# Kernel optimization log

Hardware: AMD Instinct MI355X
Metric: run time of the kernel (lower is better)

Reference implementation:

```python
import jax, jax.numpy as jnp
import numpy as np

# QP per sample: minimize c^T x + L2_REG * ||x||^2  s.t.  A x = b, lb <= x <= ub
# Solved with ADMM (splitting x = z, z in box), which is the differentiable-through-
# unrolling analogue of the SCS conic solve in the original CvxpyLayer.
L2_REG = 0.1   # config['l2_reg']
RHO = 1.0      # ADMM penalty
N_ITERS = 100  # fixed unrolled iteration count (config['diff_solver_iters'] scaled down)
JITTER = 1e-5

B, M_DIM, N_DIM = 32768, 16, 32


def setup_inputs() -> dict:
    key = jax.random.key(0)
    kA, kx, kc, kl, ku = jax.random.split(key, 5)
    A = jax.random.normal(kA, (B, M_DIM, N_DIM), jnp.float32) / np.sqrt(N_DIM)
    # feasible anchor point so the QP always has a solution
    x0 = jax.random.uniform(kx, (B, N_DIM), jnp.float32, -1.0, 1.0)
    b = jnp.einsum('bmn,bn->bm', A, x0)
    c = jax.random.normal(kc, (B, N_DIM), jnp.float32)
    lb = x0 - jax.random.uniform(kl, (B, N_DIM), jnp.float32, 0.5, 1.5)
    ub = x0 + jax.random.uniform(ku, (B, N_DIM), jnp.float32, 0.5, 1.5)
    return {"A": A, "b": b, "c": c, "lb": lb, "ub": ub}


def _solve_qp(A, b, c, lb, ub):
    sigma = 2.0 * L2_REG + RHO  # Hessian of x-subproblem is sigma*I
    m = A.shape[-2]
    # Gram matrix A A^T, inverted once per sample (small: m x m)
    M = jnp.einsum('bmn,bkn->bmk', A, A) + JITTER * jnp.eye(m, dtype=A.dtype)
    Minv = jnp.linalg.inv(M)

    def step(state, _):
        x, z, u = state
        v = RHO * (z - u) - c
        # equality-constrained x-update via KKT: x = (v - A^T nu)/sigma with A x = b
        rhs = jnp.einsum('bmn,bn->bm', A, v) - sigma * b
        nu = jnp.einsum('bmk,bk->bm', Minv, rhs)
        x = (v - jnp.einsum('bmn,bm->bn', A, nu)) / sigma
        z = jnp.clip(x + u, lb, ub)
        u = u + x - z
        return (x, z, u), None

    z0 = jnp.clip(jnp.zeros_like(c), lb, ub)
    init = (jnp.zeros_like(c), z0, jnp.zeros_like(c))
    (x, z, u), _ = jax.lax.scan(step, init, None, length=N_ITERS)
    return x


def reference(A, b, c, lb, ub):
    return _solve_qp(A, b, c, lb, ub)
```

## Files before the change

### kernel.cpp

```cpp
#include <hip/hip_runtime.h>

typedef float f16v __attribute__((ext_vector_type(16)));
typedef float f4 __attribute__((ext_vector_type(4)));
typedef float f2 __attribute__((ext_vector_type(2)));

template<int I> struct ic { static constexpr int v = I; };
template<int... I> struct iseq {};
template<int N, int... I> struct mk : mk<N-1, N-1, I...> {};
template<int... I> struct mk<0, I...> { using t = iseq<I...>; };
template<class F, int... I>
__device__ __forceinline__ void sfor_impl(F f, iseq<I...>) { (f(ic<I>{}), ...); }
template<int N, class F>
__device__ __forceinline__ void sfor(F f) { sfor_impl(f, typename mk<N>::t{}); }

namespace {
constexpr float kSigma  = 1.2f;
constexpr float kJitter = 1e-5f;
constexpr int   kIters  = 100;
constexpr int   MD = 16;
constexpr int   ND = 32;
constexpr int   SPA = 8;
constexpr int   AS  = 132;
}

__device__ __forceinline__ float4 lds_a4(const float* As, int r, int j) {
    return *reinterpret_cast<const float4*>(&As[r * 32 + ((j ^ (r & 7)) << 2)]);
}
__device__ __forceinline__ f2 lds_a2(const float* As, int r, int n) {
    return *reinterpret_cast<const f2*>(
        &As[r * 32 + ((((n >> 2) ^ (r & 7)) << 2) | (n & 3))]);
}

__global__ void __launch_bounds__(128)
admm_fused_kernel(const float* __restrict__ Ag, const float* __restrict__ bg,
                  const float* __restrict__ cg, const float* __restrict__ lbg,
                  const float* __restrict__ ubg, float* __restrict__ outg)
{
    __shared__ __align__(16) float A_lds[SPA * AS * 4];

    const int t = threadIdx.x;

    {
        const float4* src = reinterpret_cast<const float4*>(Ag) +
                            (size_t)blockIdx.x * (SPA * MD * ND / 4);
        float4* dst = reinterpret_cast<float4*>(A_lds);
        #pragma unroll
        for (int r = 0; r < 8; ++r) {
            int idx = r * 128 + t;
            int smp = idx >> 7;
            int row = (idx >> 3) & 15;
            int j   = idx & 7;
            dst[smp * AS + row * 8 + (j ^ (row & 7))] = src[idx];
        }
    }
    __syncthreads();

    const int lane = t & 63;
    const int l    = lane & 15;
    const int n0   = 2 * l;
    const int smp  = (t >> 6) * 4 + (lane >> 4);
    const size_t gs = (size_t)blockIdx.x * SPA + smp;
    const float* As = &A_lds[smp * AS * 4];

    f16v Ar0, Ar1;
    sfor<4>([&](auto J) {
        constexpr int j = decltype(J)::v;
        float4 v  = lds_a4(As, l, j);
        Ar0[4*j+0] = v.x;  Ar0[4*j+1] = v.y;  Ar0[4*j+2] = v.z;  Ar0[4*j+3] = v.w;
        float4 w4 = lds_a4(As, l, j + 4);
        Ar1[4*j+0] = w4.x; Ar1[4*j+1] = w4.y; Ar1[4*j+2] = w4.z; Ar1[4*j+3] = w4.w;
    });

    f16v Mrow, Vrow;
    sfor<16>([&](auto K) {
        constexpr int k = decltype(K)::v;
        float a0 = 0.f, a1 = 0.f, a2 = 0.f, a3 = 0.f;
        sfor<4>([&](auto J) {
            constexpr int j = decltype(J)::v;
            float4 v  = lds_a4(As, k, j);
            a0 += Ar0[4*j+0]*v.x;  a1 += Ar0[4*j+1]*v.y;
            a2 += Ar0[4*j+2]*v.z;  a3 += Ar0[4*j+3]*v.w;
            float4 w4 = lds_a4(As, k, j + 4);
            a0 += Ar1[4*j+0]*w4.x; a1 += Ar1[4*j+1]*w4.y;
            a2 += Ar1[4*j+2]*w4.z; a3 += Ar1[4*j+3]*w4.w;
        });
        Mrow[k] = (a0+a1)+(a2+a3) + ((k == l) ? kJitter : 0.f);
        Vrow[k] = (k == l) ? 1.f : 0.f;
    });

    sfor<16>([&](auto K) {
        constexpr int k = decltype(K)::v;
        float ip = 1.f / __shfl(Mrow[k], k, 16);
        float f  = (l == k) ? 0.f : Mrow[k] * ip;
        sfor<16>([&](auto J) {
            constexpr int j = decltype(J)::v;
            if constexpr (j > k) {
                float mj = __shfl(Mrow[j], k, 16);
                Mrow[j] = (l == k) ? mj * ip : Mrow[j] - f * mj;
            }
        });
        sfor<16>([&](auto J) {
            constexpr int j = decltype(J)::v;
            if constexpr (j < k) {
                float vj = __shfl(Vrow[j], k, 16);
                Vrow[j] = (l == k) ? vj * ip : Vrow[j] - f * vj;
            }
        });
        Vrow[k] = (l == k) ? ip : -f;
    });

    float w = 0.f;
    {
        float bval = bg[gs * MD + l];
        sfor<16>([&](auto K) {
            constexpr int k = decltype(K)::v;
            w += Vrow[k] * __shfl(bval, k, 16);
        });
    }

    f16v Ca = (f16v)0.0f, Cb = (f16v)0.0f;
    float q0 = 0.f, q1 = 0.f;
    sfor<16>([&](auto K) {
        constexpr int k = decltype(K)::v;
        f2 ak = lds_a2(As, k, n0);
        float wm = __shfl(w, k, 16);
        q0 = fmaf(ak[0], wm, q0);
        q1 = fmaf(ak[1], wm, q1);
        sfor<16>([&](auto M) {
            constexpr int m = decltype(M)::v;
            float mv = __shfl(Vrow[m], k, 16);
            Ca[m] = fmaf(ak[0], mv, Ca[m]);
            Cb[m] = fmaf(ak[1], mv, Cb[m]);
        });
    });

    constexpr float is = 1.f / kSigma;
#define QBUILD(j)                                                             \
    f2 Qa##j, Qb##j;                                                          \
    {                                                                         \
        const int n = 2 * ((l - (j)) & 15);                                   \
        float qa0 = 0.f, qa1 = 0.f, qb0 = 0.f, qb1 = 0.f;                     \
        sfor<16>([&](auto M) {                                                \
            constexpr int m = decltype(M)::v;                                 \
            f2 ak = lds_a2(As, m, n);                                         \
            qa0 = fmaf(Ca[m], ak[0], qa0); qa1 = fmaf(Ca[m], ak[1], qa1);     \
            qb0 = fmaf(Cb[m], ak[0], qb0); qb1 = fmaf(Cb[m], ak[1], qb1);     \
        });                                                                   \
        Qa##j[0] = ((((j) == 0) ? 1.f : 0.f) - qa0) * is;                     \
        Qa##j[1] = (0.f - qa1) * is;                                          \
        Qb##j[0] = (0.f - qb0) * is;                                          \
        Qb##j[1] = ((((j) == 0) ? 1.f : 0.f) - qb1) * is;                     \
    }
    QBUILD(0)  QBUILD(1)  QBUILD(2)  QBUILD(3)
    QBUILD(4)  QBUILD(5)  QBUILD(6)  QBUILD(7)
    QBUILD(8)  QBUILD(9)  QBUILD(10) QBUILD(11)
    QBUILD(12) QBUILD(13) QBUILD(14) QBUILD(15)
#undef QBUILD

    float d0, d1;
    {
        f2 cpr = *reinterpret_cast<const f2*>(cg + gs * ND + n0);
        float pc0 = 0.f, pc1 = 0.f;
#define DSTEP(j) {                                                            \
        const int cp = (l - (j)) & 15;                                        \
        float c0 = __shfl(cpr[0], cp, 16);                                    \
        float c1 = __shfl(cpr[1], cp, 16);                                    \
        pc0 += Qa##j[0]*c0 + Qa##j[1]*c1;                                     \
        pc1 += Qb##j[0]*c0 + Qb##j[1]*c1; }
        DSTEP(0)  DSTEP(1)  DSTEP(2)  DSTEP(3)
        DSTEP(4)  DSTEP(5)  DSTEP(6)  DSTEP(7)
        DSTEP(8)  DSTEP(9)  DSTEP(10) DSTEP(11)
        DSTEP(12) DSTEP(13) DSTEP(14) DSTEP(15)
#undef DSTEP
        d0 = q0 - pc0;
        d1 = q1 - pc1;
    }

    f2 lbv = *reinterpret_cast<const f2*>(lbg + gs * ND + n0);
    f2 ubv = *reinterpret_cast<const f2*>(ubg + gs * ND + n0);
    float lb0 = lbv[0], lb1 = lbv[1], ub0 = ubv[0], ub1 = ubv[1];
    float z0 = fminf(fmaxf(0.f, lb0), ub0);
    float z1 = fminf(fmaxf(0.f, lb1), ub1);
    float u0 = 0.f, u1 = 0.f, x0 = 0.f, x1 = 0.f;

#define FSTEP(j)                                                              \
    asm("v_fmac_f32_dpp %0, %1, %2 row_ror:" #j " row_mask:0xf bank_mask:0xf" \
        : "+v"(ae) : "v"(s0), "v"(Qa##j[0]));                                 \
    asm("v_fmac_f32_dpp %0, %1, %2 row_ror:" #j " row_mask:0xf bank_mask:0xf" \
        : "+v"(ao) : "v"(s1), "v"(Qa##j[1]));                                 \
    asm("v_fmac_f32_dpp %0, %1, %2 row_ror:" #j " row_mask:0xf bank_mask:0xf" \
        : "+v"(be) : "v"(s0), "v"(Qb##j[0]));                                 \
    asm("v_fmac_f32_dpp %0, %1, %2 row_ror:" #j " row_mask:0xf bank_mask:0xf" \
        : "+v"(bo) : "v"(s1), "v"(Qb##j[1]));

    for (int it = 0; it < kIters; ++it) {
        float s0 = z0 - u0, s1 = z1 - u1;
        float ae = d0, ao = 0.f, be = d1, bo = 0.f;
        ae = fmaf(Qa0[0], s0, ae); ao = fmaf(Qa0[1], s1, ao);
        be = fmaf(Qb0[0], s0, be); bo = fmaf(Qb0[1], s1, bo);
        FSTEP(1)  FSTEP(2)  FSTEP(3)  FSTEP(4)  FSTEP(5)
        FSTEP(6)  FSTEP(7)  FSTEP(8)  FSTEP(9)  FSTEP(10)
        FSTEP(11) FSTEP(12) FSTEP(13) FSTEP(14) FSTEP(15)
        x0 = ae + ao;
        x1 = be + bo;
        float t0 = x0 + u0, t1 = x1 + u1;
        z0 = fminf(fmaxf(t0, lb0), ub0);
        z1 = fminf(fmaxf(t1, lb1), ub1);
        u0 = t0 - z0;
        u1 = t1 - z1;
    }
#undef FSTEP

    f2 xo; xo[0] = x0; xo[1] = x1;
    *reinterpret_cast<f2*>(outg + gs * ND + n0) = xo;
}

extern "C" void kernel_launch(void* const* d_in, const int* in_sizes, int n_in,
                              void* d_out, int out_size, void* d_ws, size_t ws_size,
                              hipStream_t stream) {
    const float* A  = (const float*)d_in[0];
    const float* b  = (const float*)d_in[1];
    const float* c  = (const float*)d_in[2];
    const float* lb = (const float*)d_in[3];
    const float* ub = (const float*)d_in[4];
    float* out = (float*)d_out;
    const int B = in_sizes[1] / MD;
    admm_fused_kernel<<<B / SPA, 128, 0, stream>>>(A, b, c, lb, ub, out);
}
```

Before: 155.6 us.

## Broadcast ADMM iterate through LDS instead of DPP row rotations

```diff
diff --git a/kernel.cpp b/kernel.cpp
--- a/kernel.cpp
+++ b/kernel.cpp
@@ -134,44 +134,55 @@
         });
     });
 
+    f4 pa0=(f4)0.f, pa1=(f4)0.f, pa2=(f4)0.f, pa3=(f4)0.f,
+       pa4=(f4)0.f, pa5=(f4)0.f, pa6=(f4)0.f, pa7=(f4)0.f;
+    f4 pb0=(f4)0.f, pb1=(f4)0.f, pb2=(f4)0.f, pb3=(f4)0.f,
+       pb4=(f4)0.f, pb5=(f4)0.f, pb6=(f4)0.f, pb7=(f4)0.f;
+#define ACC4(P, c, v) \
+    P[0]=fmaf((c),(v).x,P[0]); P[1]=fmaf((c),(v).y,P[1]); \
+    P[2]=fmaf((c),(v).z,P[2]); P[3]=fmaf((c),(v).w,P[3]);
+    sfor<16>([&](auto M) {
+        constexpr int m = decltype(M)::v;
+        float c0 = Ca[m], c1 = Cb[m];
+        float4 v;
+        v = lds_a4(As, m, 0); ACC4(pa0, c0, v) ACC4(pb0, c1, v)
+        v = lds_a4(As, m, 1); ACC4(pa1, c0, v) ACC4(pb1, c1, v)
+        v = lds_a4(As, m, 2); ACC4(pa2, c0, v) ACC4(pb2, c1, v)
+        v = lds_a4(As, m, 3); ACC4(pa3, c0, v) ACC4(pb3, c1, v)
+        v = lds_a4(As, m, 4); ACC4(pa4, c0, v) ACC4(pb4, c1, v)
+        v = lds_a4(As, m, 5); ACC4(pa5, c0, v) ACC4(pb5, c1, v)
+        v = lds_a4(As, m, 6); ACC4(pa6, c0, v) ACC4(pb6, c1, v)
+        v = lds_a4(As, m, 7); ACC4(pa7, c0, v) ACC4(pb7, c1, v)
+    });
+#undef ACC4
     constexpr float is = 1.f / kSigma;
-#define QBUILD(j)                                                             \
-    f2 Qa##j, Qb##j;                                                          \
-    {                                                                         \
-        const int n = 2 * ((l - (j)) & 15);                                   \
-        float qa0 = 0.f, qa1 = 0.f, qb0 = 0.f, qb1 = 0.f;                     \
-        sfor<16>([&](auto M) {                                                \
-            constexpr int m = decltype(M)::v;                                 \
-            f2 ak = lds_a2(As, m, n);                                         \
-            qa0 = fmaf(Ca[m], ak[0], qa0); qa1 = fmaf(Ca[m], ak[1], qa1);     \
-            qb0 = fmaf(Cb[m], ak[0], qb0); qb1 = fmaf(Cb[m], ak[1], qb1);     \
-        });                                                                   \
-        Qa##j[0] = ((((j) == 0) ? 1.f : 0.f) - qa0) * is;                     \
-        Qa##j[1] = (0.f - qa1) * is;                                          \
-        Qb##j[0] = (0.f - qb0) * is;                                          \
-        Qb##j[1] = ((((j) == 0) ? 1.f : 0.f) - qb1) * is;                     \
-    }
-    QBUILD(0)  QBUILD(1)  QBUILD(2)  QBUILD(3)
-    QBUILD(4)  QBUILD(5)  QBUILD(6)  QBUILD(7)
-    QBUILD(8)  QBUILD(9)  QBUILD(10) QBUILD(11)
-    QBUILD(12) QBUILD(13) QBUILD(14) QBUILD(15)
-#undef QBUILD
+#define FIN4(P, B, R) \
+    P[0] = ((((B)+0)==(R) ? 1.f : 0.f) - P[0]) * is; \
+    P[1] = ((((B)+1)==(R) ? 1.f : 0.f) - P[1]) * is; \
+    P[2] = ((((B)+2)==(R) ? 1.f : 0.f) - P[2]) * is; \
+    P[3] = ((((B)+3)==(R) ? 1.f : 0.f) - P[3]) * is;
+    FIN4(pa0, 0,  n0) FIN4(pa1, 4,  n0) FIN4(pa2, 8,  n0) FIN4(pa3, 12, n0)
+    FIN4(pa4, 16, n0) FIN4(pa5, 20, n0) FIN4(pa6, 24, n0) FIN4(pa7, 28, n0)
+    FIN4(pb0, 0,  n0+1) FIN4(pb1, 4,  n0+1) FIN4(pb2, 8,  n0+1) FIN4(pb3, 12, n0+1)
+    FIN4(pb4, 16, n0+1) FIN4(pb5, 20, n0+1) FIN4(pb6, 24, n0+1) FIN4(pb7, 28, n0+1)
+#undef FIN4
 
     float d0, d1;
     {
-        f2 cpr = *reinterpret_cast<const f2*>(cg + gs * ND + n0);
+        float cv0 = cg[gs * ND + l];
+        float cv1 = cg[gs * ND + 16 + l];
         float pc0 = 0.f, pc1 = 0.f;
-#define DSTEP(j) {                                                            \
-        const int cp = (l - (j)) & 15;                                        \
-        float c0 = __shfl(cpr[0], cp, 16);                                    \
-        float c1 = __shfl(cpr[1], cp, 16);                                    \
-        pc0 += Qa##j[0]*c0 + Qa##j[1]*c1;                                     \
-        pc1 += Qb##j[0]*c0 + Qb##j[1]*c1; }
-        DSTEP(0)  DSTEP(1)  DSTEP(2)  DSTEP(3)
-        DSTEP(4)  DSTEP(5)  DSTEP(6)  DSTEP(7)
-        DSTEP(8)  DSTEP(9)  DSTEP(10) DSTEP(11)
-        DSTEP(12) DSTEP(13) DSTEP(14) DSTEP(15)
-#undef DSTEP
+#define DP4(PA, PB, CS, NB) { \
+        float c_; \
+        c_ = __shfl((CS), (NB)+0, 16); pc0 = fmaf(PA[0], c_, pc0); pc1 = fmaf(PB[0], c_, pc1); \
+        c_ = __shfl((CS), (NB)+1, 16); pc0 = fmaf(PA[1], c_, pc0); pc1 = fmaf(PB[1], c_, pc1); \
+        c_ = __shfl((CS), (NB)+2, 16); pc0 = fmaf(PA[2], c_, pc0); pc1 = fmaf(PB[2], c_, pc1); \
+        c_ = __shfl((CS), (NB)+3, 16); pc0 = fmaf(PA[3], c_, pc0); pc1 = fmaf(PB[3], c_, pc1); }
+        DP4(pa0, pb0, cv0, 0)  DP4(pa1, pb1, cv0, 4)
+        DP4(pa2, pb2, cv0, 8)  DP4(pa3, pb3, cv0, 12)
+        DP4(pa4, pb4, cv1, 0)  DP4(pa5, pb5, cv1, 4)
+        DP4(pa6, pb6, cv1, 8)  DP4(pa7, pb7, cv1, 12)
+#undef DP4
         d0 = q0 - pc0;
         d1 = q1 - pc1;
     }
@@ -183,33 +194,37 @@
     float z1 = fminf(fmaxf(0.f, lb1), ub1);
     float u0 = 0.f, u1 = 0.f, x0 = 0.f, x1 = 0.f;
 
-#define FSTEP(j)                                                              \
-    asm("v_fmac_f32_dpp %0, %1, %2 row_ror:" #j " row_mask:0xf bank_mask:0xf" \
-        : "+v"(ae) : "v"(s0), "v"(Qa##j[0]));                                 \
-    asm("v_fmac_f32_dpp %0, %1, %2 row_ror:" #j " row_mask:0xf bank_mask:0xf" \
-        : "+v"(ao) : "v"(s1), "v"(Qa##j[1]));                                 \
-    asm("v_fmac_f32_dpp %0, %1, %2 row_ror:" #j " row_mask:0xf bank_mask:0xf" \
-        : "+v"(be) : "v"(s0), "v"(Qb##j[0]));                                 \
-    asm("v_fmac_f32_dpp %0, %1, %2 row_ror:" #j " row_mask:0xf bank_mask:0xf" \
-        : "+v"(bo) : "v"(s1), "v"(Qb##j[1]));
+    float* Sb = const_cast<float*>(As);
+    const f4* Sv = reinterpret_cast<const f4*>(Sb);
 
     for (int it = 0; it < kIters; ++it) {
-        float s0 = z0 - u0, s1 = z1 - u1;
-        float ae = d0, ao = 0.f, be = d1, bo = 0.f;
-        ae = fmaf(Qa0[0], s0, ae); ao = fmaf(Qa0[1], s1, ao);
-        be = fmaf(Qb0[0], s0, be); bo = fmaf(Qb0[1], s1, bo);
-        FSTEP(1)  FSTEP(2)  FSTEP(3)  FSTEP(4)  FSTEP(5)
-        FSTEP(6)  FSTEP(7)  FSTEP(8)  FSTEP(9)  FSTEP(10)
-        FSTEP(11) FSTEP(12) FSTEP(13) FSTEP(14) FSTEP(15)
-        x0 = ae + ao;
-        x1 = be + bo;
+        asm volatile("" : "+v"(pa0), "+v"(pa1), "+v"(pa2), "+v"(pa3),
+                          "+v"(pa4), "+v"(pa5), "+v"(pa6), "+v"(pa7),
+                          "+v"(pb0), "+v"(pb1), "+v"(pb2), "+v"(pb3),
+                          "+v"(pb4), "+v"(pb5), "+v"(pb6), "+v"(pb7));
+        f2 sp; sp[0] = z0 - u0; sp[1] = z1 - u1;
+        *reinterpret_cast<f2*>(&Sb[2 * l]) = sp;
+        asm volatile("s_waitcnt lgkmcnt(0)" ::: "memory");
+        f4 s0 = Sv[0], s1 = Sv[1], s2 = Sv[2], s3 = Sv[3];
+        f4 s4 = Sv[4], s5 = Sv[5], s6 = Sv[6], s7 = Sv[7];
+        float a0 = d0, a1 = 0.f, a2 = 0.f, a3 = 0.f;
+        float e0 = d1, e1 = 0.f, e2 = 0.f, e3 = 0.f;
+#define XK(PA, PB, S) \
+        a0 = fmaf(PA[0], S[0], a0); a1 = fmaf(PA[1], S[1], a1); \
+        a2 = fmaf(PA[2], S[2], a2); a3 = fmaf(PA[3], S[3], a3); \
+        e0 = fmaf(PB[0], S[0], e0); e1 = fmaf(PB[1], S[1], e1); \
+        e2 = fmaf(PB[2], S[2], e2); e3 = fmaf(PB[3], S[3], e3);
+        XK(pa0, pb0, s0) XK(pa1, pb1, s1) XK(pa2, pb2, s2) XK(pa3, pb3, s3)
+        XK(pa4, pb4, s4) XK(pa5, pb5, s5) XK(pa6, pb6, s6) XK(pa7, pb7, s7)
+#undef XK
+        x0 = (a0 + a1) + (a2 + a3);
+        x1 = (e0 + e1) + (e2 + e3);
         float t0 = x0 + u0, t1 = x1 + u1;
         z0 = fminf(fmaxf(t0, lb0), ub0);
         z1 = fminf(fmaxf(t1, lb1), ub1);
         u0 = t0 - z0;
         u1 = t1 - z1;
     }
-#undef FSTEP
 
     f2 xo; xo[0] = x0; xo[1] = x1;
     *reinterpret_cast<f2*>(outg + gs * ND + n0) = xo;
```

Result: slower. 473.2 us (+204.1%).
